# Kernel tuning notes

Hardware: AMD Instinct MI355X
Metric: run time of the kernel (lower is better)

Reference implementation:

```python
import jax, jax.numpy as jnp
import numpy as np
import math

B, S, E = 2, 2048, 2048
H = 16
DH = E // H            # 128
L = 64                 # latent_dim
EB = 128               # effective block size (== block_size, adjuster init = log(block_size))
KB = 4 * EB            # kv block size = 512


def setup_inputs() -> dict:
    key = jax.random.key(0)
    ks = jax.random.split(key, 16)
    s_e = 1.0 / math.sqrt(E)
    s_dh = 1.0 / math.sqrt(DH)
    return {
        "x": jax.random.normal(ks[0], (B, S, E), jnp.float32),
        "Wq": jax.random.normal(ks[1], (E, E), jnp.float32) * s_e,
        "bq": jnp.zeros((E,), jnp.float32),
        "Wk": jax.random.normal(ks[2], (E, E), jnp.float32) * s_e,
        "bk": jnp.zeros((E,), jnp.float32),
        "Wv": jax.random.normal(ks[3], (E, E), jnp.float32) * s_e,
        "bv": jnp.zeros((E,), jnp.float32),
        "Wo": jax.random.normal(ks[4], (E, E), jnp.float32) * s_e,
        "bo": jnp.zeros((E,), jnp.float32),
        "Wql": jax.random.normal(ks[5], (DH, L), jnp.float32) * s_dh,
        "bql": jnp.zeros((L,), jnp.float32),
        "Wkl": jax.random.normal(ks[6], (DH, L), jnp.float32) * s_dh,
        "bkl": jnp.zeros((L,), jnp.float32),
        "Wm": jax.random.normal(ks[7], (DH, DH), jnp.float32) * s_dh,
        "bm": jnp.zeros((DH,), jnp.float32),
    }


def _split_heads(t):
    # [B,S,E] -> [B,H,S,DH]
    return t.reshape(B, S, H, DH).transpose(0, 2, 1, 3)


def reference(x, Wq, bq, Wk, bk, Wv, bv, Wo, bo, Wql, bql, Wkl, bkl, Wm, bm):
    q = _split_heads(x @ Wq + bq)
    k = _split_heads(x @ Wk + bk)
    v = _split_heads(x @ Wv + bv)

    # elu+1 feature maps on latent projections
    q_lat = jax.nn.elu(q @ Wql + bql) + 1.0  # [B,H,S,L]
    k_lat = jax.nn.elu(k @ Wkl + bkl) + 1.0  # [B,H,S,L]

    nq, nk = S // EB, S // KB
    qb = q_lat.reshape(B, H, nq, EB, L)
    kb = k_lat.reshape(B, H, nk, KB, L)
    vb = v.reshape(B, H, nk, KB, DH)

    scale = 1.0 / math.sqrt(L)
    # per-(q block, kv block) scores: [B,H,nq,nk,EB,KB]
    scores = jnp.einsum("bhqel,bhkfl->bhqkef", qb, kb) * scale
    # softmax independently over each kv block (axis = f), then SUM over kv blocks
    probs = jax.nn.softmax(scores, axis=-1)
    out = jnp.einsum("bhqkef,bhkfd->bhqed", probs, vb)  # [B,H,nq,EB,DH]
    out = out.reshape(B, H, S, DH)

    # latent mixer: Linear(head_dim) -> gelu
    mixed = jax.nn.gelu(out @ Wm + bm)

    y = mixed.transpose(0, 2, 1, 3).reshape(B, S, E)
    return y @ Wo + bo
```

## Files before the change

### kernel.cpp

```cpp
#include <hip/hip_runtime.h>
#include <stdint.h>
#include <math.h>

#define B_ 2
#define S_ 2048
#define E_ 2048
#define H_ 16
#define DH_ 128
#define L_ 64

typedef unsigned short u16;
typedef __attribute__((ext_vector_type(4))) float f32x4;
typedef __attribute__((ext_vector_type(8))) short short8;
typedef __attribute__((ext_vector_type(4))) short short4v;

__device__ __forceinline__ u16 f2bf(float f) {
    union { float f; uint32_t u; } c; c.f = f;
    uint32_t u = c.u + 0x7fff + ((c.u >> 16) & 1);
    return (u16)(u >> 16);
}
__device__ __forceinline__ float bf2f(u16 h) {
    union { uint32_t u; float f; } c; c.u = ((uint32_t)h) << 16;
    return c.f;
}
__device__ __forceinline__ float elu1(float x) {
    return x > 0.f ? x + 1.f : __expf(x);
}
__device__ __forceinline__ float gelu_tanh(float x) {
    float z = 0.7978845608028654f * (x + 0.044715f * x * x * x);
    float az = fabsf(z);
    float e = __expf(-2.f * az);
    float t = (1.f - e) / (1.f + e);
    t = (z >= 0.f) ? t : -t;
    return 0.5f * x * (1.f + t);
}
__device__ __forceinline__ void async16(u16* lds_dst, const u16* g_src) {
    __builtin_amdgcn_global_load_lds(
        (const __attribute__((address_space(1))) uint32_t*)g_src,
        (__attribute__((address_space(3))) uint32_t*)lds_dst, 16, 0, 0);
}
__device__ __forceinline__ int swz_off(int row, int chunk) {
    return ((chunk ^ (row & 7)) << 3);
}

__global__ __launch_bounds__(256) void cvt_bf16(const float* __restrict__ in,
                                                u16* __restrict__ out, int n8) {
    for (int i = blockIdx.x * 256 + threadIdx.x; i < n8; i += gridDim.x * 256) {
        float4 a = reinterpret_cast<const float4*>(in)[2 * i];
        float4 b = reinterpret_cast<const float4*>(in)[2 * i + 1];
        u16 u[8] __attribute__((aligned(16)));
        u[0] = f2bf(a.x); u[1] = f2bf(a.y); u[2] = f2bf(a.z); u[3] = f2bf(a.w);
        u[4] = f2bf(b.x); u[5] = f2bf(b.y); u[6] = f2bf(b.z); u[7] = f2bf(b.w);
        reinterpret_cast<int4*>(out)[i] = *(const int4*)u;
    }
}

__global__ __launch_bounds__(256) void wtrans(const float* __restrict__ W,
                                              u16* __restrict__ Wt, int K, int N) {
    __shared__ u16 t[64][68];
    const int tid = threadIdx.x;
    const int n0 = blockIdx.x * 64, k0 = blockIdx.y * 64;
    const int c4 = (tid & 15) * 4, r = tid >> 4;
    #pragma unroll
    for (int i = 0; i < 4; i++) {
        int row = r + 16 * i;
        float4 v = *reinterpret_cast<const float4*>(&W[(size_t)(k0 + row) * N + n0 + c4]);
        t[c4 + 0][row] = f2bf(v.x); t[c4 + 1][row] = f2bf(v.y);
        t[c4 + 2][row] = f2bf(v.z); t[c4 + 3][row] = f2bf(v.w);
    }
    __syncthreads();
    #pragma unroll
    for (int i = 0; i < 4; i++) {
        int nr = r + 16 * i;
        ushort4 o = *reinterpret_cast<const ushort4*>(&t[nr][c4]);
        *reinterpret_cast<ushort4*>(&Wt[(size_t)(n0 + nr) * K + k0 + c4]) = o;
    }
}

__global__ __launch_bounds__(256) void beff_kernel(
    const float* __restrict__ b, const float* __restrict__ Wl,
    const float* __restrict__ bl, float* __restrict__ beff, int outoff)
{
    int t = blockIdx.x * 256 + threadIdx.x;
    if (t >= 1024) return;
    int h = t >> 6, n = t & 63;
    float s = bl[n];
    for (int d = 0; d < 128; d++) s += b[h * 128 + d] * Wl[d * 64 + n];
    beff[outoff + t] = s;
}

__global__ __launch_bounds__(256) void bveff_kernel(
    const float* __restrict__ bv, const float* __restrict__ Wm,
    float* __restrict__ bveff)
{
    int t = blockIdx.x * 256 + threadIdx.x;
    if (t >= 2048) return;
    int h = t >> 7, n = t & 127;
    float s = 0.f;
    for (int d = 0; d < 128; d++) s += bv[h * 128 + d] * Wm[d * 128 + n];
    bveff[t] = s;
}

__global__ __launch_bounds__(256) void weff_kernel(
    const float* __restrict__ W, const u16* __restrict__ Wlt,
    u16* __restrict__ Wefft, int outoff)
{
    __shared__ u16 lds[8192 + 16384];
    const int tid = threadIdx.x, l = tid & 63, w = tid >> 6;
    const int k0 = blockIdx.x * 128, h = blockIdx.y;

    #pragma unroll
    for (int i = 0; i < 4; i++) {
        int lin = i * 256 + tid, row = lin >> 4, c = lin & 15;
        async16(&lds[lin * 8], &Wlt[row * 128 + swz_off(row, c)]);
    }
    #pragma unroll
    for (int i = 0; i < 16; i++) {
        int e = (i * 256 + tid) * 4;
        int row = e >> 7, ec = e & 127;
        float4 v4 = *reinterpret_cast<const float4*>(
            &W[(size_t)(k0 + row) * E_ + h * DH_ + ec]);
        u16 u[4] __attribute__((aligned(8)));
        u[0] = f2bf(v4.x); u[1] = f2bf(v4.y); u[2] = f2bf(v4.z); u[3] = f2bf(v4.w);
        int chunk = ec >> 3, half = (ec >> 2) & 1;
        *reinterpret_cast<uint64_t*>(
            &lds[8192 + row * 128 + swz_off(row, chunk) + half * 4]) = *(const uint64_t*)u;
    }
    __syncthreads();

    f32x4 zero = {0.f, 0.f, 0.f, 0.f};
    f32x4 acc[8];
    #pragma unroll
    for (int nt = 0; nt < 8; nt++) acc[nt] = zero;
    #pragma unroll
    for (int ks = 0; ks < 4; ks++) {
        int arow = 16 * w + (l & 15);
        short8 af = *reinterpret_cast<const short8*>(
            &lds[arow * 128 + swz_off(arow, ks * 4 + (l >> 4))]);
        #pragma unroll
        for (int nt = 0; nt < 8; nt++) {
            int brow = 16 * nt + (l & 15);
            short8 bf = *reinterpret_cast<const short8*>(
                &lds[8192 + brow * 128 + swz_off(brow, ks * 4 + (l >> 4))]);
            acc[nt] = __builtin_amdgcn_mfma_f32_16x16x32_bf16(af, bf, acc[nt], 0, 0, 0);
        }
    }
    #pragma unroll
    for (int nt = 0; nt < 8; nt++) {
        int kc = k0 + 16 * nt + (l & 15);
        #pragma unroll
        for (int j = 0; j < 4; j++) {
            int nl = 16 * w + (l >> 4) * 4 + j;
            Wefft[(size_t)(outoff + h * 64 + nl) * E_ + kc] = f2bf(acc[nt][j]);
        }
    }
}

__global__ __launch_bounds__(256) void weffv_kernel(
    const float* __restrict__ Wv, const u16* __restrict__ Wmt,
    u16* __restrict__ Wv2t)
{
    __shared__ u16 lds[16384 + 16384];
    const int tid = threadIdx.x, l = tid & 63, w = tid >> 6;
    const int e0 = blockIdx.x * 128, h = blockIdx.y;

    #pragma unroll
    for (int i = 0; i < 8; i++) {
        int lin = i * 256 + tid, row = lin >> 4, c = lin & 15;
        async16(&lds[lin * 8], &Wmt[row * 128 + swz_off(row, c)]);
    }
    #pragma unroll
    for (int i = 0; i < 16; i++) {
        int e = (i * 256 + tid) * 4;
        int row = e >> 7, ec = e & 127;
        float4 v4 = *reinterpret_cast<const float4*>(
            &Wv[(size_t)(e0 + row) * E_ + h * DH_ + ec]);
        u16 u[4] __attribute__((aligned(8)));
        u[0] = f2bf(v4.x); u[1] = f2bf(v4.y); u[2] = f2bf(v4.z); u[3] = f2bf(v4.w);
        int chunk = ec >> 3, half = (ec >> 2) & 1;
        *reinterpret_cast<uint64_t*>(
            &lds[16384 + row * 128 + swz_off(row, chunk) + half * 4]) = *(const uint64_t*)u;
    }
    __syncthreads();

    f32x4 zero = {0.f, 0.f, 0.f, 0.f};
    f32x4 acc[2][8];
    #pragma unroll
    for (int mi = 0; mi < 2; mi++)
        #pragma unroll
        for (int nt = 0; nt < 8; nt++) acc[mi][nt] = zero;
    #pragma unroll
    for (int ks = 0; ks < 4; ks++) {
        short8 af[2];
        #pragma unroll
        for (int mi = 0; mi < 2; mi++) {
            int arow = 32 * w + 16 * mi + (l & 15);
            af[mi] = *reinterpret_cast<const short8*>(
                &lds[arow * 128 + swz_off(arow, ks * 4 + (l >> 4))]);
        }
        #pragma unroll
        for (int nt = 0; nt < 8; nt++) {
            int brow = 16 * nt + (l & 15);
            short8 bf = *reinterpret_cast<const short8*>(
                &lds[16384 + brow * 128 + swz_off(brow, ks * 4 + (l >> 4))]);
            #pragma unroll
            for (int mi = 0; mi < 2; mi++)
                acc[mi][nt] = __builtin_amdgcn_mfma_f32_16x16x32_bf16(af[mi], bf, acc[mi][nt], 0, 0, 0);
        }
    }
    #pragma unroll
    for (int mi = 0; mi < 2; mi++)
        #pragma unroll
        for (int nt = 0; nt < 8; nt++) {
            int ec = e0 + 16 * nt + (l & 15);
            #pragma unroll
            for (int j = 0; j < 4; j++) {
                int dp = 32 * w + 16 * mi + (l >> 4) * 4 + j;
                Wv2t[(size_t)(h * 128 + dp) * E_ + ec] = f2bf(acc[mi][nt][j]);
            }
        }
}

template <typename OutT, bool DUAL, int EPI>
__global__ __launch_bounds__(256) void gemm_bf16(
    const u16* __restrict__ A, const u16* __restrict__ A2,
    const u16* __restrict__ Wt, const float* __restrict__ bias,
    OutT* __restrict__ C, u16* __restrict__ latq, u16* __restrict__ latk,
    int M, int N, int K)
{
    __shared__ u16 lds[DUAL ? 24576 : 16384];
    const int tid = threadIdx.x, l = tid & 63, w = tid >> 6;
    const int wr = w >> 1, wc = w & 1;
    const int row0 = blockIdx.y * 128, col0 = blockIdx.x * 128;

    f32x4 zero = {0.f, 0.f, 0.f, 0.f};
    f32x4 acc[4][4];
    #pragma unroll
    for (int i = 0; i < 4; i++)
        #pragma unroll
        for (int j = 0; j < 4; j++) acc[i][j] = zero;

    for (int k0 = 0; k0 < K; k0 += 64) {
        #pragma unroll
        for (int i = 0; i < 4; i++) {
            int lin = i * 256 + tid, row = lin >> 3, c = lin & 7;
            int sc = swz_off(row, c);
            async16(&lds[lin * 8], &A[(size_t)(row0 + row) * K + k0 + sc]);
            async16(&lds[8192 + lin * 8], &Wt[(size_t)(col0 + row) * K + k0 + sc]);
            if (DUAL) async16(&lds[16384 + lin * 8], &A2[(size_t)(row0 + row) * K + k0 + sc]);
        }
        __syncthreads();
        #pragma unroll
        for (int ks = 0; ks < 2; ks++) {
            short8 af[4], bf[4], af2[4];
            #pragma unroll
            for (int mi = 0; mi < 4; mi++) {
                int row = 64 * wr + 16 * mi + (l & 15);
                int idx = row * 64 + swz_off(row, ks * 4 + (l >> 4));
                af[mi] = *reinterpret_cast<const short8*>(&lds[idx]);
                if (DUAL) af2[mi] = *reinterpret_cast<const short8*>(&lds[16384 + idx]);
            }
            #pragma unroll
            for (int ni = 0; ni < 4; ni++) {
                int row = 64 * wc + 16 * ni + (l & 15);
                int idx = 8192 + row * 64 + swz_off(row, ks * 4 + (l >> 4));
                bf[ni] = *reinterpret_cast<const short8*>(&lds[idx]);
            }
            #pragma unroll
            for (int mi = 0; mi < 4; mi++)
                #pragma unroll
                for (int ni = 0; ni < 4; ni++) {
                    acc[mi][ni] = __builtin_amdgcn_mfma_f32_16x16x32_bf16(
                        af[mi], bf[ni], acc[mi][ni], 0, 0, 0);
                    if (DUAL)
                        acc[mi][ni] = __builtin_amdgcn_mfma_f32_16x16x32_bf16(
                            af2[mi], bf[ni], acc[mi][ni], 0, 0, 0);
                }
        }
        __syncthreads();
    }
    #pragma unroll
    for (int mi = 0; mi < 4; mi++)
        #pragma unroll
        for (int ni = 0; ni < 4; ni++) {
            int col = col0 + 64 * wc + 16 * ni + (l & 15);
            float bv = (EPI == 2) ? 0.f : bias[col];
            #pragma unroll
            for (int j = 0; j < 4; j++) {
                int row = row0 + 64 * wr + 16 * mi + (l >> 4) * 4 + j;
                float v = acc[mi][ni][j] + ((EPI == 2) ? bias[row] : bv);
                if (EPI == 1) {
                    v = elu1(v);
                    u16* dst = (col < 1024) ? latq : latk;
                    int h = (col >> 6) & 15, n = col & 63;
                    int bb = row >> 11, s = row & 2047;
                    dst[(((size_t)bb * 16 + h) * S_ + s) * 64 + n] = f2bf(v);
                } else if (EPI == 2) {
                    int d = row & 127, hh = row >> 7;
                    int bb = col >> 11, s = col & 2047;
                    ((u16*)C)[((size_t)((bb << 4) + hh) * 128 + d) * (size_t)S_ + s] = f2bf(v);
                } else if (sizeof(OutT) == 2) {
                    C[(size_t)row * N + col] = (OutT)f2bf(v);
                } else {
                    C[(size_t)row * N + col] = (OutT)v;
                }
            }
        }
}

__global__ __launch_bounds__(256, 2) void attn_mfma(
    const u16* __restrict__ qlat, const u16* __restrict__ klat,
    const u16* __restrict__ Vt, const float* __restrict__ bm,
    u16* __restrict__ mixed)
{
    __shared__ u16 pool[32768];
    const int tid = threadIdx.x, l = tid & 63, w = tid >> 6;
    const int g = l >> 4;
    const int qi = blockIdx.x, bh = blockIdx.y;
    const int bb = bh >> 4, h = bh & 15;
    const u16* klat_bh = klat + (size_t)bh * S_ * L_;
    const u16* vt_bh = Vt + (size_t)bh * 128 * S_;
    const int q0 = qi * 128;

    #pragma unroll
    for (int i = 0; i < 4; i++) {
        int lin = i * 256 + tid, row = lin >> 3, c = lin & 7;
        async16(&pool[lin * 8],
                &qlat[((size_t)bh * S_ + q0 + row) * 64 + swz_off(row, c)]);
    }
    #pragma unroll
    for (int i = 0; i < 2; i++) {
        int lin = i * 256 + tid, row = lin >> 3, c = lin & 7;
        async16(&pool[8192 + lin * 8], &klat_bh[(size_t)row * 64 + swz_off(row, c)]);
    }
    #pragma unroll
    for (int i = 0; i < 4; i++) {
        int lin = i * 256 + tid, d = lin >> 3, c = lin & 7;
        async16(&pool[16384 + lin * 8], &vt_bh[(size_t)d * S_ + swz_off(d, c)]);
    }
    __syncthreads();

    short8 qf[2][2];
    #pragma unroll
    for (int qt = 0; qt < 2; qt++)
        #pragma unroll
        for (int ks = 0; ks < 2; ks++) {
            int row = 32 * w + 16 * qt + (l & 15);
            qf[qt][ks] = *reinterpret_cast<const short8*>(
                &pool[row * 64 + swz_off(row, ks * 4 + g)]);
        }

    f32x4 zero = {0.f, 0.f, 0.f, 0.f};
    f32x4 Ot[8][2], Op[8][2];
    float m_reg[2], l_reg[2];
    #pragma unroll
    for (int nd = 0; nd < 8; nd++)
        #pragma unroll
        for (int qt = 0; qt < 2; qt++) { Ot[nd][qt] = zero; Op[nd][qt] = zero; }
    #pragma unroll
    for (int qt = 0; qt < 2; qt++) { m_reg[qt] = -1e30f; l_reg[qt] = 0.f; }

    for (int t = 0; t < 32; t++) {
        const int cur = t & 1;
        if (t < 31) {
            const int f0 = (t + 1) * 64, nb = cur ^ 1;
            #pragma unroll
            for (int i = 0; i < 2; i++) {
                int lin = i * 256 + tid, row = lin >> 3, c = lin & 7;
                async16(&pool[8192 + nb * 4096 + lin * 8],
                        &klat_bh[(size_t)(f0 + row) * 64 + swz_off(row, c)]);
            }
            #pragma unroll
            for (int i = 0; i < 4; i++) {
                int lin = i * 256 + tid, d = lin >> 3, c = lin & 7;
                async16(&pool[16384 + nb * 8192 + lin * 8],
                        &vt_bh[(size_t)d * S_ + f0 + swz_off(d, c)]);
            }
        }
        const u16* Kb = &pool[8192 + cur * 4096];
        const u16* Vb = &pool[16384 + cur * 8192];

        f32x4 accS[4][2];
        #pragma unroll
        for (int fi = 0; fi < 4; fi++)
            #pragma unroll
            for (int qt = 0; qt < 2; qt++) accS[fi][qt] = zero;
        #pragma unroll
        for (int ks = 0; ks < 2; ks++) {
            short8 kfrag[4];
            #pragma unroll
            for (int fi = 0; fi < 4; fi++) {
                int row = 16 * fi + (l & 15);
                kfrag[fi] = *reinterpret_cast<const short8*>(
                    &Kb[row * 64 + swz_off(row, ks * 4 + g)]);
            }
            #pragma unroll
            for (int fi = 0; fi < 4; fi++)
                #pragma unroll
                for (int qt = 0; qt < 2; qt++)
                    accS[fi][qt] = __builtin_amdgcn_mfma_f32_16x16x32_bf16(
                        kfrag[fi], qf[qt][ks], accS[fi][qt], 0, 0, 0);
        }

        short4v pf[2][4];
        #pragma unroll
        for (int qt = 0; qt < 2; qt++) {
            float mx = accS[0][qt][0];
            #pragma unroll
            for (int fi = 0; fi < 4; fi++)
                #pragma unroll
                for (int j = 0; j < 4; j++) mx = fmaxf(mx, accS[fi][qt][j]);
            mx *= 0.125f;
            mx = fmaxf(mx, __shfl_xor(mx, 16));
            mx = fmaxf(mx, __shfl_xor(mx, 32));
            float mo = m_reg[qt];
            float mn = fmaxf(mo, mx);
            m_reg[qt] = mn;
            float alpha = __expf(mo - mn);
            float sum = 0.f;
            #pragma unroll
            for (int fi = 0; fi < 4; fi++) {
                float p[4];
                #pragma unroll
                for (int j = 0; j < 4; j++) {
                    p[j] = __expf(accS[fi][qt][j] * 0.125f - mn);
                    sum += p[j];
                }
                short4v pk;
                pk[0] = (short)f2bf(p[0]); pk[1] = (short)f2bf(p[1]);
                pk[2] = (short)f2bf(p[2]); pk[3] = (short)f2bf(p[3]);
                pf[qt][fi] = pk;
            }
            sum += __shfl_xor(sum, 16);
            sum += __shfl_xor(sum, 32);
            l_reg[qt] = l_reg[qt] * alpha + sum;
            if (__any(mx > mo)) {
                #pragma unroll
                for (int nd = 0; nd < 8; nd++) Op[nd][qt] *= alpha;
            }
        }

        #pragma unroll
        for (int kt = 0; kt < 4; kt++) {
            int fl = 16 * kt + 4 * g;
            int fch = fl >> 3, fsub = fl & 7;
            #pragma unroll
            for (int nd = 0; nd < 8; nd++) {
                int d = 16 * nd + (l & 15);
                short4v vfrag = *reinterpret_cast<const short4v*>(
                    &Vb[d * 64 + ((fch ^ (d & 7)) << 3) + fsub]);
                #pragma unroll
                for (int qt = 0; qt < 2; qt++)
                    Op[nd][qt] = __builtin_amdgcn_mfma_f32_16x16x16bf16_1k(
                        vfrag, pf[qt][kt], Op[nd][qt], 0, 0, 0);
            }
        }

        if ((t & 7) == 7) {
            #pragma unroll
            for (int qt = 0; qt < 2; qt++) {
                float linv = 1.f / l_reg[qt];
                #pragma unroll
                for (int nd = 0; nd < 8; nd++) {
                    Ot[nd][qt] += Op[nd][qt] * linv;
                    Op[nd][qt] = zero;
                }
                m_reg[qt] = -1e30f; l_reg[qt] = 0.f;
            }
        }
        __syncthreads();
    }

    #pragma unroll
    for (int nd = 0; nd < 8; nd++)
        #pragma unroll
        for (int qt = 0; qt < 2; qt++) {
            int q = q0 + 32 * w + 16 * qt + (l & 15);
            u16 hi4[4] __attribute__((aligned(8)));
            #pragma unroll
            for (int j = 0; j < 4; j++) {
                int d = 16 * nd + 4 * g + j;
                float v = gelu_tanh(Ot[nd][qt][j] + bm[d]);
                hi4[j] = f2bf(v);
            }
            size_t o = ((size_t)(bb * S_ + q)) * E_ + h * DH_ + 16 * nd + 4 * g;
            *reinterpret_cast<ushort4*>(&mixed[o]) = *(const ushort4*)hi4;
        }
}

extern "C" void kernel_launch(void* const* d_in, const int* in_sizes, int n_in,
                              void* d_out, int out_size, void* d_ws, size_t ws_size,
                              hipStream_t stream)
{
    const float* x   = (const float*)d_in[0];
    const float* Wq  = (const float*)d_in[1];
    const float* bq  = (const float*)d_in[2];
    const float* Wk  = (const float*)d_in[3];
    const float* bk  = (const float*)d_in[4];
    const float* Wv  = (const float*)d_in[5];
    const float* bv  = (const float*)d_in[6];
    const float* Wo  = (const float*)d_in[7];
    const float* bo  = (const float*)d_in[8];
    const float* Wql = (const float*)d_in[9];
    const float* bql = (const float*)d_in[10];
    const float* Wkl = (const float*)d_in[11];
    const float* bkl = (const float*)d_in[12];
    const float* Wm  = (const float*)d_in[13];
    const float* bm  = (const float*)d_in[14];
    float* out = (float*)d_out;

    u16* ws0   = (u16*)d_ws;
    u16* xb    = ws0;
    u16* Wefft = ws0 + 8388608;
    u16* Wv2t  = Wefft + 4194304;
    u16* Wot   = Wv2t + 4194304;
    u16* Wmt   = Wot + 4194304;
    u16* Wqlt  = Wmt + 16384;
    u16* Wklt  = Wqlt + 8192;
    float* beff  = (float*)(Wklt + 8192);
    float* bveff = beff + 2048;
    u16* Vt    = (u16*)(bveff + 2048);
    u16* qlat  = Vt + 8388608;
    u16* klat  = qlat + 4194304;
    u16* mixed = xb;

    dim3 gemm_g(16, 32);
    dim3 gemmv_g(32, 16);
    dim3 head_g(16, 32);

    cvt_bf16<<<2048, 256, 0, stream>>>(x, xb, 1048576);
    wtrans<<<dim3(32, 32), 256, 0, stream>>>(Wo, Wot, 2048, 2048);
    wtrans<<<dim3(2, 2), 256, 0, stream>>>(Wm, Wmt, 128, 128);
    wtrans<<<dim3(1, 2), 256, 0, stream>>>(Wql, Wqlt, 128, 64);
    wtrans<<<dim3(1, 2), 256, 0, stream>>>(Wkl, Wklt, 128, 64);
    beff_kernel<<<4, 256, 0, stream>>>(bq, Wql, bql, beff, 0);
    beff_kernel<<<4, 256, 0, stream>>>(bk, Wkl, bkl, beff, 1024);
    bveff_kernel<<<8, 256, 0, stream>>>(bv, Wm, bveff);
    weff_kernel<<<dim3(16, 16), 256, 0, stream>>>(Wq, Wqlt, Wefft, 0);
    weff_kernel<<<dim3(16, 16), 256, 0, stream>>>(Wk, Wklt, Wefft, 1024);
    weffv_kernel<<<dim3(16, 16), 256, 0, stream>>>(Wv, Wmt, Wv2t);

    gemm_bf16<u16, false, 1><<<gemm_g, 256, 0, stream>>>(
        xb, nullptr, Wefft, beff, (u16*)nullptr, qlat, klat, 4096, 2048, 2048);
    gemm_bf16<u16, false, 2><<<gemmv_g, 256, 0, stream>>>(
        Wv2t, nullptr, xb, bveff, Vt, nullptr, nullptr, 2048, 4096, 2048);
    attn_mfma<<<head_g, 256, 0, stream>>>(qlat, klat, Vt, bm, mixed);
    gemm_bf16<float, false, 0><<<gemm_g, 256, 0, stream>>>(
        mixed, nullptr, Wot, bo, out, nullptr, nullptr, 4096, 2048, 2048);
}
```

Measured before the change: 281.1 us.

## Halve attention query tile to 64 rows, raise occupancy, add MFMA priority hints

```diff
diff --git a/kernel.cpp b/kernel.cpp
--- a/kernel.cpp
+++ b/kernel.cpp
@@ -18,6 +18,10 @@
     union { float f; uint32_t u; } c; c.f = f;
     uint32_t u = c.u + 0x7fff + ((c.u >> 16) & 1);
     return (u16)(u >> 16);
+}
+__device__ __forceinline__ u16 f2bf_ru(float f) {
+    union { float f; uint32_t u; } c; c.f = f;
+    return (u16)((c.u + 0x8000u) >> 16);
 }
 __device__ __forceinline__ float bf2f(u16 h) {
     union { uint32_t u; float f; } c; c.u = ((uint32_t)h) << 16;
@@ -308,57 +312,52 @@
         }
 }
 
-__global__ __launch_bounds__(256, 2) void attn_mfma(
+__global__ __launch_bounds__(256, 3) void attn_mfma(
     const u16* __restrict__ qlat, const u16* __restrict__ klat,
     const u16* __restrict__ Vt, const float* __restrict__ bm,
     u16* __restrict__ mixed)
 {
-    __shared__ u16 pool[32768];
+    __shared__ u16 pool[24576];
     const int tid = threadIdx.x, l = tid & 63, w = tid >> 6;
     const int g = l >> 4;
     const int qi = blockIdx.x, bh = blockIdx.y;
     const int bb = bh >> 4, h = bh & 15;
     const u16* klat_bh = klat + (size_t)bh * S_ * L_;
     const u16* vt_bh = Vt + (size_t)bh * 128 * S_;
-    const int q0 = qi * 128;
-
-    #pragma unroll
-    for (int i = 0; i < 4; i++) {
-        int lin = i * 256 + tid, row = lin >> 3, c = lin & 7;
-        async16(&pool[lin * 8],
-                &qlat[((size_t)bh * S_ + q0 + row) * 64 + swz_off(row, c)]);
-    }
+    const int q0 = qi * 64;
+
     #pragma unroll
     for (int i = 0; i < 2; i++) {
         int lin = i * 256 + tid, row = lin >> 3, c = lin & 7;
-        async16(&pool[8192 + lin * 8], &klat_bh[(size_t)row * 64 + swz_off(row, c)]);
+        async16(&pool[4096 + lin * 8],
+                &qlat[((size_t)bh * S_ + q0 + row) * 64 + swz_off(row, c)]);
+    }
+    #pragma unroll
+    for (int i = 0; i < 2; i++) {
+        int lin = i * 256 + tid, row = lin >> 3, c = lin & 7;
+        async16(&pool[lin * 8], &klat_bh[(size_t)row * 64 + swz_off(row, c)]);
     }
     #pragma unroll
     for (int i = 0; i < 4; i++) {
         int lin = i * 256 + tid, d = lin >> 3, c = lin & 7;
-        async16(&pool[16384 + lin * 8], &vt_bh[(size_t)d * S_ + swz_off(d, c)]);
+        async16(&pool[8192 + lin * 8], &vt_bh[(size_t)d * S_ + swz_off(d, c)]);
     }
     __syncthreads();
 
-    short8 qf[2][2];
-    #pragma unroll
-    for (int qt = 0; qt < 2; qt++)
-        #pragma unroll
-        for (int ks = 0; ks < 2; ks++) {
-            int row = 32 * w + 16 * qt + (l & 15);
-            qf[qt][ks] = *reinterpret_cast<const short8*>(
-                &pool[row * 64 + swz_off(row, ks * 4 + g)]);
-        }
+    short8 qf[2];
+    #pragma unroll
+    for (int ks = 0; ks < 2; ks++) {
+        int row = 16 * w + (l & 15);
+        qf[ks] = *reinterpret_cast<const short8*>(
+            &pool[4096 + row * 64 + swz_off(row, ks * 4 + g)]);
+    }
+    __syncthreads();
 
     f32x4 zero = {0.f, 0.f, 0.f, 0.f};
-    f32x4 Ot[8][2], Op[8][2];
-    float m_reg[2], l_reg[2];
-    #pragma unroll
-    for (int nd = 0; nd < 8; nd++)
-        #pragma unroll
-        for (int qt = 0; qt < 2; qt++) { Ot[nd][qt] = zero; Op[nd][qt] = zero; }
-    #pragma unroll
-    for (int qt = 0; qt < 2; qt++) { m_reg[qt] = -1e30f; l_reg[qt] = 0.f; }
+    f32x4 Ot[8], Op[8];
+    float m_reg = -1e30f, l_reg = 0.f;
+    #pragma unroll
+    for (int nd = 0; nd < 8; nd++) { Ot[nd] = zero; Op[nd] = zero; }
 
     for (int t = 0; t < 32; t++) {
         const int cur = t & 1;
@@ -367,24 +366,22 @@
             #pragma unroll
             for (int i = 0; i < 2; i++) {
                 int lin = i * 256 + tid, row = lin >> 3, c = lin & 7;
-                async16(&pool[8192 + nb * 4096 + lin * 8],
+                async16(&pool[nb * 4096 + lin * 8],
                         &klat_bh[(size_t)(f0 + row) * 64 + swz_off(row, c)]);
             }
             #pragma unroll
             for (int i = 0; i < 4; i++) {
                 int lin = i * 256 + tid, d = lin >> 3, c = lin & 7;
-                async16(&pool[16384 + nb * 8192 + lin * 8],
+                async16(&pool[8192 + nb * 8192 + lin * 8],
                         &vt_bh[(size_t)d * S_ + f0 + swz_off(d, c)]);
             }
         }
-        const u16* Kb = &pool[8192 + cur * 4096];
-        const u16* Vb = &pool[16384 + cur * 8192];
-
-        f32x4 accS[4][2];
-        #pragma unroll
-        for (int fi = 0; fi < 4; fi++)
-            #pragma unroll
-            for (int qt = 0; qt < 2; qt++) accS[fi][qt] = zero;
+        const u16* Kb = &pool[cur * 4096];
+        const u16* Vb = &pool[8192 + cur * 8192];
+
+        f32x4 accS[4];
+        #pragma unroll
+        for (int fi = 0; fi < 4; fi++) accS[fi] = zero;
         #pragma unroll
         for (int ks = 0; ks < 2; ks++) {
             short8 kfrag[4];
@@ -394,28 +391,29 @@
                 kfrag[fi] = *reinterpret_cast<const short8*>(
                     &Kb[row * 64 + swz_off(row, ks * 4 + g)]);
             }
+            __builtin_amdgcn_s_setprio(1);
             #pragma unroll
             for (int fi = 0; fi < 4; fi++)
-                #pragma unroll
-                for (int qt = 0; qt < 2; qt++)
-                    accS[fi][qt] = __builtin_amdgcn_mfma_f32_16x16x32_bf16(
-                        kfrag[fi], qf[qt][ks], accS[fi][qt], 0, 0, 0);
-        }
-
-        short4v pf[2][4];
-        #pragma unroll
-        for (int qt = 0; qt < 2; qt++) {
-            float mx = accS[0][qt][0];
-            #pragma unroll
-            for (int fi = 0; fi < 4; fi++)
-                #pragma unroll
-                for (int j = 0; j < 4; j++) mx = fmaxf(mx, accS[fi][qt][j]);
+                accS[fi] = __builtin_amdgcn_mfma_f32_16x16x32_bf16(
+                    kfrag[fi], qf[ks], accS[fi], 0, 0, 0);
+            __builtin_amdgcn_s_setprio(0);
+        }
+
+        short4v pf[4];
+        {
+            float mx = fmaxf(fmaxf(accS[0][0], accS[0][1]), fmaxf(accS[0][2], accS[0][3]));
+            #pragma unroll
+            for (int fi = 1; fi < 4; fi++) {
+                float m2 = fmaxf(fmaxf(accS[fi][0], accS[fi][1]),
+                                 fmaxf(accS[fi][2], accS[fi][3]));
+                mx = fmaxf(mx, m2);
+            }
             mx *= 0.125f;
             mx = fmaxf(mx, __shfl_xor(mx, 16));
             mx = fmaxf(mx, __shfl_xor(mx, 32));
-            float mo = m_reg[qt];
+            float mo = m_reg;
             float mn = fmaxf(mo, mx);
-            m_reg[qt] = mn;
+            m_reg = mn;
             float alpha = __expf(mo - mn);
             float sum = 0.f;
             #pragma unroll
@@ -423,20 +421,20 @@
                 float p[4];
                 #pragma unroll
                 for (int j = 0; j < 4; j++) {
-                    p[j] = __expf(accS[fi][qt][j] * 0.125f - mn);
+                    p[j] = __expf(accS[fi][j] * 0.125f - mn);
                     sum += p[j];
                 }
                 short4v pk;
-                pk[0] = (short)f2bf(p[0]); pk[1] = (short)f2bf(p[1]);
-                pk[2] = (short)f2bf(p[2]); pk[3] = (short)f2bf(p[3]);
-                pf[qt][fi] = pk;
+                pk[0] = (short)f2bf_ru(p[0]); pk[1] = (short)f2bf_ru(p[1]);
+                pk[2] = (short)f2bf_ru(p[2]); pk[3] = (short)f2bf_ru(p[3]);
+                pf[fi] = pk;
             }
             sum += __shfl_xor(sum, 16);
             sum += __shfl_xor(sum, 32);
-            l_reg[qt] = l_reg[qt] * alpha + sum;
+            l_reg = l_reg * alpha + sum;
             if (__any(mx > mo)) {
                 #pragma unroll
-                for (int nd = 0; nd < 8; nd++) Op[nd][qt] *= alpha;
+                for (int nd = 0; nd < 8; nd++) Op[nd] *= alpha;
             }
         }
 
@@ -444,48 +442,43 @@
         for (int kt = 0; kt < 4; kt++) {
             int fl = 16 * kt + 4 * g;
             int fch = fl >> 3, fsub = fl & 7;
+            __builtin_amdgcn_s_setprio(1);
             #pragma unroll
             for (int nd = 0; nd < 8; nd++) {
                 int d = 16 * nd + (l & 15);
                 short4v vfrag = *reinterpret_cast<const short4v*>(
                     &Vb[d * 64 + ((fch ^ (d & 7)) << 3) + fsub]);
-                #pragma unroll
-                for (int qt = 0; qt < 2; qt++)
-                    Op[nd][qt] = __builtin_amdgcn_mfma_f32_16x16x16bf16_1k(
-                        vfrag, pf[qt][kt], Op[nd][qt], 0, 0, 0);
-            }
+                Op[nd] = __builtin_amdgcn_mfma_f32_16x16x16bf16_1k(
+                    vfrag, pf[kt], Op[nd], 0, 0, 0);
+            }
+            __builtin_amdgcn_s_setprio(0);
         }
 
         if ((t & 7) == 7) {
-            #pragma unroll
-            for (int qt = 0; qt < 2; qt++) {
-                float linv = 1.f / l_reg[qt];
-                #pragma unroll
-                for (int nd = 0; nd < 8; nd++) {
-                    Ot[nd][qt] += Op[nd][qt] * linv;
-                    Op[nd][qt] = zero;
-                }
-                m_reg[qt] = -1e30f; l_reg[qt] = 0.f;
-            }
+            float linv = 1.f / l_reg;
+            #pragma unroll
+            for (int nd = 0; nd < 8; nd++) {
+                Ot[nd] += Op[nd] * linv;
+                Op[nd] = zero;
+            }
+            m_reg = -1e30f; l_reg = 0.f;
         }
         __syncthreads();
     }
 
     #pragma unroll
-    for (int nd = 0; nd < 8; nd++)
-        #pragma unroll
-        for (int qt = 0; qt < 2; qt++) {
-            int q = q0 + 32 * w + 16 * qt + (l & 15);
-            u16 hi4[4] __attribute__((aligned(8)));
-            #pragma unroll
-            for (int j = 0; j < 4; j++) {
-                int d = 16 * nd + 4 * g + j;
-                float v = gelu_tanh(Ot[nd][qt][j] + bm[d]);
-                hi4[j] = f2bf(v);
-            }
-            size_t o = ((size_t)(bb * S_ + q)) * E_ + h * DH_ + 16 * nd + 4 * g;
-            *reinterpret_cast<ushort4*>(&mixed[o]) = *(const ushort4*)hi4;
-        }
+    for (int nd = 0; nd < 8; nd++) {
+        int q = q0 + 16 * w + (l & 15);
+        u16 hi4[4] __attribute__((aligned(8)));
+        #pragma unroll
+        for (int j = 0; j < 4; j++) {
+            int d = 16 * nd + 4 * g + j;
+            float v = gelu_tanh(Ot[nd][j] + bm[d]);
+            hi4[j] = f2bf(v);
+        }
+        size_t o = ((size_t)(bb * S_ + q)) * E_ + h * DH_ + 16 * nd + 4 * g;
+        *reinterpret_cast<ushort4*>(&mixed[o]) = *(const ushort4*)hi4;
+    }
 }
 
 extern "C" void kernel_launch(void* const* d_in, const int* in_sizes, int n_in,
@@ -526,7 +519,7 @@
 
     dim3 gemm_g(16, 32);
     dim3 gemmv_g(32, 16);
-    dim3 head_g(16, 32);
+    dim3 attn_g(32, 32);
 
     cvt_bf16<<<2048, 256, 0, stream>>>(x, xb, 1048576);
     wtrans<<<dim3(32, 32), 256, 0, stream>>>(Wo, Wot, 2048, 2048);
@@ -544,7 +537,7 @@
         xb, nullptr, Wefft, beff, (u16*)nullptr, qlat, klat, 4096, 2048, 2048);
     gemm_bf16<u16, false, 2><<<gemmv_g, 256, 0, stream>>>(
         Wv2t, nullptr, xb, bveff, Vt, nullptr, nullptr, 2048, 4096, 2048);
-    attn_mfma<<<head_g, 256, 0, stream>>>(qlat, klat, Vt, bm, mixed);
+    attn_mfma<<<attn_g, 256, 0, stream>>>(qlat, klat, Vt, bm, mixed);
     gemm_bf16<float, false, 0><<<gemm_g, 256, 0, stream>>>(
         mixed, nullptr, Wot, bo, out, nullptr, nullptr, 4096, 2048, 2048);
 }
```

Result: slower. 308.2 us (+9.7%).

## Load V fragments directly from global into registers in attention kernel

Applied to the files above, without the earlier changes.

```diff
diff --git a/kernel.cpp b/kernel.cpp
--- a/kernel.cpp
+++ b/kernel.cpp
@@ -18,6 +18,10 @@
     union { float f; uint32_t u; } c; c.f = f;
     uint32_t u = c.u + 0x7fff + ((c.u >> 16) & 1);
     return (u16)(u >> 16);
+}
+__device__ __forceinline__ u16 f2bf_ru(float f) {
+    union { float f; uint32_t u; } c; c.f = f;
+    return (u16)((c.u + 0x8000u) >> 16);
 }
 __device__ __forceinline__ float bf2f(u16 h) {
     union { uint32_t u; float f; } c; c.u = ((uint32_t)h) << 16;
@@ -313,7 +317,7 @@
     const u16* __restrict__ Vt, const float* __restrict__ bm,
     u16* __restrict__ mixed)
 {
-    __shared__ u16 pool[32768];
+    __shared__ u16 pool[16384];
     const int tid = threadIdx.x, l = tid & 63, w = tid >> 6;
     const int g = l >> 4;
     const int qi = blockIdx.x, bh = blockIdx.y;
@@ -333,11 +337,6 @@
         int lin = i * 256 + tid, row = lin >> 3, c = lin & 7;
         async16(&pool[8192 + lin * 8], &klat_bh[(size_t)row * 64 + swz_off(row, c)]);
     }
-    #pragma unroll
-    for (int i = 0; i < 4; i++) {
-        int lin = i * 256 + tid, d = lin >> 3, c = lin & 7;
-        async16(&pool[16384 + lin * 8], &vt_bh[(size_t)d * S_ + swz_off(d, c)]);
-    }
     __syncthreads();
 
     short8 qf[2][2];
@@ -350,6 +349,11 @@
                 &pool[row * 64 + swz_off(row, ks * 4 + g)]);
         }
 
+    const u16* vp[8];
+    #pragma unroll
+    for (int nd = 0; nd < 8; nd++)
+        vp[nd] = vt_bh + (size_t)(16 * nd + (l & 15)) * S_ + 4 * g;
+
     f32x4 zero = {0.f, 0.f, 0.f, 0.f};
     f32x4 Ot[8][2], Op[8][2];
     float m_reg[2], l_reg[2];
@@ -362,23 +366,24 @@
 
     for (int t = 0; t < 32; t++) {
         const int cur = t & 1;
+        const int f0 = t * 64;
         if (t < 31) {
-            const int f0 = (t + 1) * 64, nb = cur ^ 1;
+            const int fn = (t + 1) * 64, nb = cur ^ 1;
             #pragma unroll
             for (int i = 0; i < 2; i++) {
                 int lin = i * 256 + tid, row = lin >> 3, c = lin & 7;
                 async16(&pool[8192 + nb * 4096 + lin * 8],
-                        &klat_bh[(size_t)(f0 + row) * 64 + swz_off(row, c)]);
-            }
-            #pragma unroll
-            for (int i = 0; i < 4; i++) {
-                int lin = i * 256 + tid, d = lin >> 3, c = lin & 7;
-                async16(&pool[16384 + nb * 8192 + lin * 8],
-                        &vt_bh[(size_t)d * S_ + f0 + swz_off(d, c)]);
+                        &klat_bh[(size_t)(fn + row) * 64 + swz_off(row, c)]);
             }
         }
         const u16* Kb = &pool[8192 + cur * 4096];
-        const u16* Vb = &pool[16384 + cur * 8192];
+
+        short4v vfrag[4][8];
+        #pragma unroll
+        for (int kt = 0; kt < 4; kt++)
+            #pragma unroll
+            for (int nd = 0; nd < 8; nd++)
+                vfrag[kt][nd] = *reinterpret_cast<const short4v*>(vp[nd] + f0 + 16 * kt);
 
         f32x4 accS[4][2];
         #pragma unroll
@@ -394,12 +399,14 @@
                 kfrag[fi] = *reinterpret_cast<const short8*>(
                     &Kb[row * 64 + swz_off(row, ks * 4 + g)]);
             }
+            __builtin_amdgcn_s_setprio(1);
             #pragma unroll
             for (int fi = 0; fi < 4; fi++)
                 #pragma unroll
                 for (int qt = 0; qt < 2; qt++)
                     accS[fi][qt] = __builtin_amdgcn_mfma_f32_16x16x32_bf16(
                         kfrag[fi], qf[qt][ks], accS[fi][qt], 0, 0, 0);
+            __builtin_amdgcn_s_setprio(0);
         }
 
         short4v pf[2][4];
@@ -427,8 +434,8 @@
                     sum += p[j];
                 }
                 short4v pk;
-                pk[0] = (short)f2bf(p[0]); pk[1] = (short)f2bf(p[1]);
-                pk[2] = (short)f2bf(p[2]); pk[3] = (short)f2bf(p[3]);
+                pk[0] = (short)f2bf_ru(p[0]); pk[1] = (short)f2bf_ru(p[1]);
+                pk[2] = (short)f2bf_ru(p[2]); pk[3] = (short)f2bf_ru(p[3]);
                 pf[qt][fi] = pk;
             }
             sum += __shfl_xor(sum, 16);
@@ -442,18 +449,14 @@
 
         #pragma unroll
         for (int kt = 0; kt < 4; kt++) {
-            int fl = 16 * kt + 4 * g;
-            int fch = fl >> 3, fsub = fl & 7;
-            #pragma unroll
-            for (int nd = 0; nd < 8; nd++) {
-                int d = 16 * nd + (l & 15);
-                short4v vfrag = *reinterpret_cast<const short4v*>(
-                    &Vb[d * 64 + ((fch ^ (d & 7)) << 3) + fsub]);
+            __builtin_amdgcn_s_setprio(1);
+            #pragma unroll
+            for (int nd = 0; nd < 8; nd++)
                 #pragma unroll
                 for (int qt = 0; qt < 2; qt++)
                     Op[nd][qt] = __builtin_amdgcn_mfma_f32_16x16x16bf16_1k(
-                        vfrag, pf[qt][kt], Op[nd][qt], 0, 0, 0);
-            }
+                        vfrag[kt][nd], pf[qt][kt], Op[nd][qt], 0, 0, 0);
+            __builtin_amdgcn_s_setprio(0);
         }
 
         if ((t & 7) == 7) {
@@ -526,7 +529,7 @@
 
     dim3 gemm_g(16, 32);
     dim3 gemmv_g(32, 16);
-    dim3 head_g(16, 32);
+    dim3 attn_g(16, 32);
 
     cvt_bf16<<<2048, 256, 0, stream>>>(x, xb, 1048576);
     wtrans<<<dim3(32, 32), 256, 0, stream>>>(Wo, Wot, 2048, 2048);
@@ -544,7 +547,7 @@
         xb, nullptr, Wefft, beff, (u16*)nullptr, qlat, klat, 4096, 2048, 2048);
     gemm_bf16<u16, false, 2><<<gemmv_g, 256, 0, stream>>>(
         Wv2t, nullptr, xb, bveff, Vt, nullptr, nullptr, 2048, 4096, 2048);
-    attn_mfma<<<head_g, 256, 0, stream>>>(qlat, klat, Vt, bm, mixed);
+    attn_mfma<<<attn_g, 256, 0, stream>>>(qlat, klat, Vt, bm, mixed);
     gemm_bf16<float, false, 0><<<gemm_g, 256, 0, stream>>>(
         mixed, nullptr, Wot, bo, out, nullptr, nullptr, 4096, 2048, 2048);
 }
```

Measured after the change: 474.8 us. +68.9%, slower.
